# Performance work log

Measured on AMD Instinct MI355X. Metric: run time of the kernel, lower is better.

## Reference

```python
import jax, jax.numpy as jnp
import numpy as np

V = 32          # num_variables
T = 48          # num_time_bins
D = 512         # d_model
H = 8           # num_heads
HD = D // H     # head_dim = 64
OD = 16         # observation_dim
B = 4


def setup_inputs() -> dict:
    key = jax.random.key(0)
    ks = jax.random.split(key, 20)
    s = 0.02
    inp = {
        'h': jax.random.normal(ks[0], (B, T, V, D), jnp.float32),
        'observation_state': jax.random.normal(ks[1], (B, T, V, 2), jnp.float32),
        'Wq': jax.random.normal(ks[2], (D, D), jnp.float32) * s,
        'bq': jnp.zeros((D,), jnp.float32),
        'Wk': jax.random.normal(ks[3], (D, D), jnp.float32) * s,
        'bk': jnp.zeros((D,), jnp.float32),
        'Wv': jax.random.normal(ks[4], (D, D), jnp.float32) * s,
        'bv': jnp.zeros((D,), jnp.float32),
        'Wo': jax.random.normal(ks[5], (D, D), jnp.float32) * s,
        'bo': jnp.zeros((D,), jnp.float32),
        'Woq': jax.random.normal(ks[6], (2, H * OD), jnp.float32) * 0.5,
        'boq': jnp.zeros((H * OD,), jnp.float32),
        'Wok': jax.random.normal(ks[7], (2, H * OD), jnp.float32) * 0.5,
        'bok': jnp.zeros((H * OD,), jnp.float32),
        'variable_bias': jax.random.normal(ks[8], (H, V, V), jnp.float32) * 0.01,
        'relative_time_bias': jax.random.normal(ks[9], (H, 2 * T - 1), jnp.float32) * 0.01,
    }
    return inp


def reference(h, observation_state, Wq, bq, Wk, bk, Wv, bv, Wo, bo,
              Woq, boq, Wok, bok, variable_bias, relative_time_bias):
    N = T * V
    scale = 1.0 / np.sqrt(HD)
    obs_scale = 1.0 / np.sqrt(OD)

    # static index buffers (constants)
    flat_var_ids = jnp.tile(jnp.arange(V), T)                       # [N]
    flat_time_ids = jnp.repeat(jnp.arange(T), V)                    # [N]
    rel_index = flat_time_ids[:, None] - flat_time_ids[None, :] + (T - 1)  # [N,N]

    fh = h.reshape(B, N, D)
    fo = observation_state.reshape(B, N, 2)

    def heads(x, nh, hd):
        return x.reshape(B, N, nh, hd).transpose(0, 2, 1, 3)  # [B,H,N,hd]

    q = heads(fh @ Wq + bq, H, HD)
    k = heads(fh @ Wk + bk, H, HD)
    v = heads(fh @ Wv + bv, H, HD)
    oq = heads(fo @ Woq + boq, H, OD)
    ok = heads(fo @ Wok + bok, H, OD)

    content = jnp.einsum('bhnd,bhmd->bhnm', q, k) * scale
    obs = jnp.einsum('bhnd,bhmd->bhnm', oq, ok) * obs_scale
    var_scores = variable_bias[:, flat_var_ids[:, None], flat_var_ids[None, :]]  # [H,N,N]
    time_scores = relative_time_bias[:, rel_index]                                # [H,N,N]

    scores = content + obs + var_scores[None] + time_scores[None]
    attn = jax.nn.softmax(scores, axis=-1)  # dropout off (inference)
    out = jnp.einsum('bhnm,bhmd->bhnd', attn, v)
    out = out.transpose(0, 2, 1, 3).reshape(B, N, D)
    out = out @ Wo + bo
    return out.reshape(B, T, V, D)
```

## Files before the change

### kernel.cpp

```cpp
#include <hip/hip_runtime.h>
#include <math.h>

typedef __bf16 bf16x8 __attribute__((ext_vector_type(8)));
typedef float f32x4 __attribute__((ext_vector_type(4)));

#define NB 4
#define NT 48
#define NV 32
#define ND 512
#define NH 8
#define NN 1536
#define NBN 6144
#define L2E 1.44269504f

#define GLOAD_LDS(g, l) \
    __builtin_amdgcn_global_load_lds( \
        (const __attribute__((address_space(1))) void*)(g), \
        (__attribute__((address_space(3))) void*)(l), 16, 0, 0)

__global__ __launch_bounds__(256) void prep(
    const float* __restrict__ h, const float* __restrict__ obs,
    const float* __restrict__ Wq, const float* __restrict__ Wk,
    const float* __restrict__ Wv, const float* __restrict__ Wo,
    const float* __restrict__ bq, const float* __restrict__ bk,
    const float* __restrict__ bv,
    const float* __restrict__ Wok, const float* __restrict__ bok,
    __bf16* __restrict__ h_bf, __bf16* __restrict__ WcatT,
    __bf16* __restrict__ WoT, float* __restrict__ biascat,
    __bf16* __restrict__ kx)
{
    __shared__ float ts[64][68];
    const int tid = threadIdx.x;
    const int bx = blockIdx.x;
    if (bx < 1536) {
        int t = bx * 256 + tid;
        const float4* src = (const float4*)h + (size_t)t * 2;
        float4 a = src[0], b = src[1];
        __bf16 r[8] = {(__bf16)a.x, (__bf16)a.y, (__bf16)a.z, (__bf16)a.w,
                       (__bf16)b.x, (__bf16)b.y, (__bf16)b.z, (__bf16)b.w};
        *(uint4*)(h_bf + (size_t)t * 8) = *(uint4*)r;
    } else if (bx < 1792) {
        int bw = bx - 1536;
        const int p = bw >> 6, tile = bw & 63;
        const int k0 = (tile >> 3) * 64, c0 = (tile & 7) * 64;
        const float* W = (p == 0) ? Wq : (p == 1) ? Wk : (p == 2) ? Wv : Wo;
        const float scale = (p == 0) ? 0.125f * L2E : 1.0f;
        #pragma unroll
        for (int i = 0; i < 4; i++) {
            int r = (tid >> 4) + i * 16;
            float4 v = *(const float4*)(W + (size_t)(k0 + r) * 512 + c0 + (tid & 15) * 4);
            *(float4*)&ts[r][(tid & 15) * 4] = v;
        }
        __syncthreads();
        __bf16 tmp[16];
        #pragma unroll
        for (int j = 0; j < 16; j++)
            tmp[j] = (__bf16)(ts[(tid & 3) * 16 + j][tid >> 2] * scale);
        int crow = c0 + (tid >> 2);
        __bf16* dst = (p < 3)
            ? WcatT + ((size_t)(p * 512 + crow)) * 512 + k0 + (tid & 3) * 16
            : WoT   + ((size_t)crow) * 512 + k0 + (tid & 3) * 16;
        *(uint4*)dst = *(uint4*)tmp;
        *(uint4*)(dst + 8) = *(uint4*)(tmp + 8);
        if (p < 3 && k0 == 0 && tid < 64) {
            const float* bb = (p == 0) ? bq : (p == 1) ? bk : bv;
            biascat[p * 512 + c0 + tid] = bb[c0 + tid] * scale;
        }
    } else {
        int t = (bx - 1792) * 256 + tid;
        int row = t >> 1, half = t & 1;
        __bf16* dst = kx + (size_t)row * 96 + 64 + half * 16;
        if (half == 0) {
            int bh = row / NN, n = row - bh * NN;
            int b = bh >> 3, hh = bh & 7;
            size_t bn = (size_t)b * NN + n;
            float o0 = obs[bn * 2], o1 = obs[bn * 2 + 1];
            int f = hh * 16;
            __bf16 tmp[16];
            #pragma unroll
            for (int j = 0; j < 16; j++)
                tmp[j] = (__bf16)(o0 * Wok[f + j] + o1 * Wok[128 + f + j] + bok[f + j]);
            *(uint4*)dst       = *(uint4*)tmp;
            *(uint4*)(dst + 8) = *(uint4*)(tmp + 8);
        } else {
            uint4 z = {0, 0, 0, 0};
            *(uint4*)dst       = z;
            *(uint4*)(dst + 8) = z;
        }
    }
}

template<int TM, bool BF16OUT>
__global__ __launch_bounds__(256) void gemm_mfma(
    const __bf16* __restrict__ A, const __bf16* __restrict__ Bt,
    const float* __restrict__ bias, float* __restrict__ Cf,
    __bf16* __restrict__ qarr, __bf16* __restrict__ kx,
    __bf16* __restrict__ vt)
{
    constexpr int MT = TM / 32;
    __shared__ __align__(16) char smem[34816];
    char* const As0 = smem;
    char* const As1 = smem + TM * 64;
    char* const Bs0 = smem + TM * 128;
    char* const Bs1 = smem + TM * 128 + 8192;
    const int tid = threadIdx.x;
    const int w = tid >> 6, lane = tid & 63;
    const int quad = lane >> 4, l16 = lane & 15;
    const int wm = w >> 1, wn = w & 1;
    const int n0 = blockIdx.x * 128, m0 = blockIdx.y * TM;

    const int sm = tid >> 2;
    const int sk = ((tid & 3) ^ ((sm >> 1) & 3)) * 8;
    const __bf16* aptr = A  + (size_t)(m0 + sm) * 512 + sk;
    const __bf16* bptr = Bt + (size_t)(n0 + sm) * 512 + sk;

    f32x4 zero4 = {0.f, 0.f, 0.f, 0.f};
    f32x4 acc[MT][4];
    #pragma unroll
    for (int i = 0; i < MT; i++)
        #pragma unroll
        for (int j = 0; j < 4; j++) acc[i][j] = zero4;

    auto STAGE = [&](char* dA, char* dB, int kt) {
        GLOAD_LDS(aptr + kt, dA + tid * 16);
        if (TM == 128) GLOAD_LDS(aptr + 64 * 512 + kt, dA + 4096 + tid * 16);
        GLOAD_LDS(bptr + kt, dB + tid * 16);
        GLOAD_LDS(bptr + 64 * 512 + kt, dB + 4096 + tid * 16);
    };
    auto COMPUTE = [&](const char* Asb, const char* Bsb) {
        bf16x8 af[MT], bfr[4];
        #pragma unroll
        for (int mt = 0; mt < MT; mt++) {
            int rr = wm * (TM / 2) + mt * 16 + l16;
            af[mt] = *(const bf16x8*)(Asb + rr * 64 + (quad ^ ((rr >> 1) & 3)) * 16);
        }
        #pragma unroll
        for (int nt = 0; nt < 4; nt++) {
            int rr = wn * 64 + nt * 16 + l16;
            bfr[nt] = *(const bf16x8*)(Bsb + rr * 64 + (quad ^ ((rr >> 1) & 3)) * 16);
        }
        #pragma unroll
        for (int mt = 0; mt < MT; mt++)
            #pragma unroll
            for (int nt = 0; nt < 4; nt++)
                acc[mt][nt] = __builtin_amdgcn_mfma_f32_16x16x32_bf16(
                    af[mt], bfr[nt], acc[mt][nt], 0, 0, 0);
    };

    STAGE(As0, Bs0, 0);
    asm volatile("s_waitcnt vmcnt(0)" ::: "memory");
    __builtin_amdgcn_s_barrier();
    for (int kt = 0; kt < 512; kt += 64) {
        STAGE(As1, Bs1, kt + 32);
        COMPUTE(As0, Bs0);
        asm volatile("s_waitcnt vmcnt(0)" ::: "memory");
        __builtin_amdgcn_s_barrier();
        if (kt + 64 < 512) STAGE(As0, Bs0, kt + 64);
        COMPUTE(As1, Bs1);
        asm volatile("s_waitcnt vmcnt(0)" ::: "memory");
        __builtin_amdgcn_s_barrier();
    }

    __syncthreads();
    if (BF16OUT) {
        if (n0 >= 1024) {
            __bf16* CsT = (__bf16*)smem;
            #pragma unroll
            for (int nt = 0; nt < 4; nt++) {
                int cl = wn * 64 + nt * 16 + l16;
                float bia = bias[n0 + cl];
                #pragma unroll
                for (int mt = 0; mt < MT; mt++) {
                    int rl0 = wm * (TM / 2) + mt * 16 + quad * 4;
                    __bf16 pk[4];
                    #pragma unroll
                    for (int r = 0; r < 4; r++)
                        pk[r] = (__bf16)(acc[mt][nt][r] + bia);
                    *(uint2*)&CsT[cl * 136 + rl0] = *(uint2*)pk;
                }
            }
            __syncthreads();
            int cl = tid >> 1, half = tid & 1;
            int f0 = (n0 + cl) & 511;
            int hh = f0 >> 6, d = f0 & 63;
            int bidx = m0 / NN, nm = m0 - bidx * NN;
            __bf16* dst = vt + ((size_t)(bidx * 8 + hh) * 64 + d) * 1536
                             + nm + half * 64;
            #pragma unroll
            for (int j = 0; j < 8; j++) {
                uint4 v = *(uint4*)&CsT[cl * 136 + half * 64 + j * 8];
                *(uint4*)(dst + j * 8) = v;
            }
        } else {
            __bf16* Cs = (__bf16*)smem;
            #pragma unroll
            for (int mt = 0; mt < MT; mt++)
                #pragma unroll
                for (int nt = 0; nt < 4; nt++) {
                    int cl = wn * 64 + nt * 16 + l16;
                    float bia = bias[n0 + cl];
                    #pragma unroll
                    for (int r = 0; r < 4; r++) {
                        int rl = wm * (TM / 2) + mt * 16 + quad * 4 + r;
                        Cs[rl * 132 + cl] = (__bf16)(acc[mt][nt][r] + bia);
                    }
                }
            __syncthreads();
            int rl = tid >> 1, hb = tid & 1;
            int grow = m0 + rl;
            int col0 = n0 + hb * 64;
            int p = col0 >> 9, f0 = col0 & 511, hh = f0 >> 6;
            int bidx = grow / NN, n = grow - bidx * NN;
            __bf16* dst = (p == 0) ? qarr + (size_t)grow * 512 + f0
                                   : kx + ((size_t)(bidx * 8 + hh) * NN + n) * 96;
            #pragma unroll
            for (int j = 0; j < 8; j++) {
                uint2 lo = *(uint2*)&Cs[rl * 132 + hb * 64 + j * 8];
                uint2 hi = *(uint2*)&Cs[rl * 132 + hb * 64 + j * 8 + 4];
                uint4 v = {lo.x, lo.y, hi.x, hi.y};
                *(uint4*)(dst + j * 8) = v;
            }
        }
    } else {
        float* Csf = (float*)smem;
        #pragma unroll
        for (int mt = 0; mt < MT; mt++)
            #pragma unroll
            for (int nt = 0; nt < 4; nt++) {
                int cl = wn * 64 + nt * 16 + l16;
                float bia = bias[n0 + cl];
                #pragma unroll
                for (int r = 0; r < 4; r++) {
                    int rl = wm * (TM / 2) + mt * 16 + quad * 4 + r;
                    Csf[rl * 132 + cl] = acc[mt][nt][r] + bia;
                }
            }
        __syncthreads();
        int rl = tid >> 2, q4 = tid & 3;
        float* dst = Cf + (size_t)(m0 + rl) * 512 + n0 + q4 * 32;
        #pragma unroll
        for (int j = 0; j < 8; j++) {
            uint4 v = *(uint4*)&Csf[rl * 132 + q4 * 32 + j * 4];
            *(uint4*)(dst + j * 4) = v;
        }
    }
}

__global__ __launch_bounds__(256) void attn_mfma(
    const __bf16* __restrict__ qarr, const __bf16* __restrict__ kx,
    const __bf16* __restrict__ vt, const float* __restrict__ obs,
    const float* __restrict__ Woq, const float* __restrict__ boq,
    const float* __restrict__ varb, const float* __restrict__ rtb,
    __bf16* __restrict__ aout)
{
    __shared__ __align__(16) __bf16 Ks0[64][128];
    __shared__ __align__(16) __bf16 Ks1[64][128];
    __shared__ __align__(16) __bf16 Vs0[64][64];
    __shared__ __align__(16) __bf16 Vs1[64][64];
    __shared__ __align__(16) __bf16 Ps[64][64];
    __shared__ float rts[96];

    const int tid = threadIdx.x;
    const int w = tid >> 6, lane = tid & 63;
    const int quad = lane >> 4, l16 = lane & 15;
    const int bh = blockIdx.x, qt = blockIdx.y;
    const int b = bh >> 3, h = bh & 7;
    const int n0 = qt * 64;

    if (tid < 95) rts[tid] = rtb[h * 95 + tid] * L2E;

    const int ck = (tid & 15) ^ ((tid >> 4) & 7);
    const __bf16* kbase = kx + (size_t)bh * NN * 96 + ck * 8;
    const int cv = (tid & 7) ^ ((tid >> 3) & 7);
    const __bf16* vbase = vt + (size_t)bh * 64 * 1536 + cv * 8;

    auto STAGE = [&](char* dk, char* dv, int m0s) {
        #pragma unroll
        for (int i = 0; i < 4; i++) {
            int row = i * 16 + (tid >> 4);
            GLOAD_LDS(kbase + (size_t)(m0s + row) * 96, dk + i * 4096 + tid * 16);
        }
        #pragma unroll
        for (int i = 0; i < 2; i++) {
            int row = i * 32 + (tid >> 3);
            GLOAD_LDS(vbase + (size_t)row * 1536 + m0s, dv + i * 4096 + tid * 16);
        }
    };

    STAGE((char*)Ks0, (char*)Vs0, 0);

    const int nl = w * 16 + l16;
    const size_t qrow = (size_t)(b * NN + n0 + nl);
    bf16x8 bq_[3];
    bq_[0] = *(const bf16x8*)(qarr + qrow * 512 + h * 64 + quad * 8);
    bq_[1] = *(const bf16x8*)(qarr + qrow * 512 + h * 64 + 32 + quad * 8);
    {
        uint4 a2u = {0u, 0u, 0u, 0u};
        if (quad < 2) {
            float o0 = obs[qrow * 2], o1 = obs[qrow * 2 + 1];
            int f = h * 16 + quad * 8;
            const float sc = 0.25f * L2E;
            __bf16 tmp[8];
            #pragma unroll
            for (int j = 0; j < 8; j++)
                tmp[j] = (__bf16)(sc * (o0 * Woq[f + j] + o1 * Woq[128 + f + j]
                                        + boq[f + j]));
            a2u = *(uint4*)tmp;
        }
        bq_[2] = *(bf16x8*)&a2u;
    }

    const int rm = (w & 1) * 16 + l16;
    float4 vbA = *(const float4*)(varb + h * 1024 + rm * 32 + quad * 4);
    float4 vbB = *(const float4*)(varb + h * 1024 + rm * 32 + 16 + quad * 4);
    float vA[4] = {vbA.x * L2E, vbA.y * L2E, vbA.z * L2E, vbA.w * L2E};
    float vB[4] = {vbB.x * L2E, vbB.y * L2E, vbB.z * L2E, vbB.w * L2E};
    const int tn = 2 * qt + (w >> 1);

    int wo2[4], ro2[2];
    #pragma unroll
    for (int ct = 0; ct < 4; ct++)
        wo2[ct] = (((ct * 2 + (quad >> 1)) ^ (nl & 7)) * 16) + (quad & 1) * 8;
    #pragma unroll
    for (int ks = 0; ks < 2; ks++)
        ro2[ks] = ((ks * 4 + quad) ^ (nl & 7)) * 16;
    char* psrow = (char*)Ps + nl * 128;

    f32x4 zero4 = {0.f, 0.f, 0.f, 0.f};
    f32x4 o[4];
    f32x4 lpv = zero4;
    #pragma unroll
    for (int i = 0; i < 4; i++) o[i] = zero4;

    auto COMPUTE = [&](const char* Kb, const char* Vb, int mti) {
        f32x4 sc[4];
        __builtin_amdgcn_s_setprio(1);
        #pragma unroll
        for (int ct = 0; ct < 4; ct++) {
            f32x4 d = zero4;
            int row = ct * 16 + l16;
            #pragma unroll
            for (int ks = 0; ks < 3; ks++) {
                bf16x8 kf = *(const bf16x8*)(Kb + row * 256
                                + (((ks * 4 + quad) ^ (row & 7)) * 16));
                d = __builtin_amdgcn_mfma_f32_16x16x32_bf16(kf, bq_[ks], d, 0, 0, 0);
            }
            sc[ct] = d;
        }
        __builtin_amdgcn_s_setprio(0);
        float tb0 = rts[tn - 2 * mti + 47];
        float tb1 = rts[tn - 2 * mti + 46];
        #pragma unroll
        for (int ct = 0; ct < 4; ct++) {
            float tb = (ct & 2) ? tb1 : tb0;
            const float* vv = (ct & 1) ? vB : vA;
            __bf16 pk[4];
            #pragma unroll
            for (int r = 0; r < 4; r++) {
                float p = exp2f(sc[ct][r] + tb + vv[r]);
                lpv[r] += p;
                pk[r] = (__bf16)p;
            }
            *(uint2*)(psrow + wo2[ct]) = *(uint2*)pk;
        }
        __builtin_amdgcn_s_setprio(1);
        #pragma unroll
        for (int ks = 0; ks < 2; ks++) {
            bf16x8 pf = *(const bf16x8*)(psrow + ro2[ks]);
            #pragma unroll
            for (int dt = 0; dt < 4; dt++) {
                int rw = dt * 16 + l16;
                bf16x8 vf = *(const bf16x8*)(Vb + rw * 128
                                + (((ks * 4 + quad) ^ (rw & 7)) * 16));
                o[dt] = __builtin_amdgcn_mfma_f32_16x16x32_bf16(vf, pf, o[dt], 0, 0, 0);
            }
        }
        __builtin_amdgcn_s_setprio(0);
    };

    asm volatile("s_waitcnt vmcnt(0) lgkmcnt(0)" ::: "memory");
    __builtin_amdgcn_s_barrier();

    for (int mt = 0; mt < 24; mt += 2) {
        STAGE((char*)Ks1, (char*)Vs1, (mt + 1) * 64);
        COMPUTE((const char*)Ks0, (const char*)Vs0, mt);
        asm volatile("s_waitcnt vmcnt(0)" ::: "memory");
        __builtin_amdgcn_s_barrier();
        if (mt + 2 < 24) STAGE((char*)Ks0, (char*)Vs0, (mt + 2) * 64);
        COMPUTE((const char*)Ks1, (const char*)Vs1, mt + 1);
        asm volatile("s_waitcnt vmcnt(0)" ::: "memory");
        __builtin_amdgcn_s_barrier();
    }

    float lp = (lpv[0] + lpv[1]) + (lpv[2] + lpv[3]);
    lp += __shfl_xor(lp, 16);
    lp += __shfl_xor(lp, 32);
    float inv = 1.0f / lp;
    size_t abase = ((size_t)b * NN + n0 + nl) * 512 + h * 64 + quad * 4;
    #pragma unroll
    for (int dt = 0; dt < 4; dt++) {
        __bf16 ov[4];
        #pragma unroll
        for (int r = 0; r < 4; r++) ov[r] = (__bf16)(o[dt][r] * inv);
        *(uint2*)(aout + abase + dt * 16) = *(uint2*)ov;
    }
}

extern "C" void kernel_launch(void* const* d_in, const int* in_sizes, int n_in,
                              void* d_out, int out_size, void* d_ws, size_t ws_size,
                              hipStream_t stream)
{
    const float* h_   = (const float*)d_in[0];
    const float* obs  = (const float*)d_in[1];
    const float* Wq   = (const float*)d_in[2];
    const float* bq   = (const float*)d_in[3];
    const float* Wk   = (const float*)d_in[4];
    const float* bk   = (const float*)d_in[5];
    const float* Wv   = (const float*)d_in[6];
    const float* bv   = (const float*)d_in[7];
    const float* Wo   = (const float*)d_in[8];
    const float* bo   = (const float*)d_in[9];
    const float* Woq  = (const float*)d_in[10];
    const float* boq  = (const float*)d_in[11];
    const float* Wok  = (const float*)d_in[12];
    const float* bok  = (const float*)d_in[13];
    const float* varb = (const float*)d_in[14];
    const float* rtb  = (const float*)d_in[15];
    float* out = (float*)d_out;

    char* ws = (char*)d_ws;
    __bf16* h_bf    = (__bf16*)ws;                 ws += (size_t)NBN * 512 * 2;
    __bf16* qarr    = (__bf16*)ws;                 ws += (size_t)NBN * 512 * 2;
    __bf16* vt      = (__bf16*)ws;                 ws += (size_t)NBN * 512 * 2;
    __bf16* kx      = (__bf16*)ws;                 ws += ((size_t)32 * NN * 96 + 64) * 2;
    __bf16* attnout = (__bf16*)ws;                 ws += (size_t)NBN * 512 * 2;
    __bf16* WcatT   = (__bf16*)ws;                 ws += (size_t)1536 * 512 * 2;
    __bf16* WoT     = (__bf16*)ws;                 ws += (size_t)512 * 512 * 2;
    float*  biascat = (float*)ws;                  ws += 1536 * 4;

    prep<<<dim3(2176), dim3(256), 0, stream>>>(
        h_, obs, Wq, Wk, Wv, Wo, bq, bk, bv, Wok, bok,
        h_bf, WcatT, WoT, biascat, kx);
    gemm_mfma<128, true><<<dim3(12, 48), dim3(256), 0, stream>>>(
        h_bf, WcatT, biascat, nullptr, qarr, kx, vt);
    attn_mfma<<<dim3(32, 24), dim3(256), 0, stream>>>(qarr, kx, vt, obs, Woq, boq,
                                                      varb, rtb, attnout);
    gemm_mfma<64, false><<<dim3(4, 96), dim3(256), 0, stream>>>(
        attnout, WoT, bo, out, nullptr, nullptr, nullptr);
}
```

Measured before the change: 190.2 us.

## Single-buffer K tile in attention and issue next-tile loads after QK phase

Drops the second K shared-memory buffer and keeps double buffering only for V. The next K/V tile load is now issued after the QK MFMA phase and a barrier, instead of at the start of each iteration. This cuts LDS use by 16KB per block, which may allow more resident blocks per CU. In exchange it adds a barrier per tile and shortens the window in which the K load can overlap compute.

```diff
diff --git a/kernel.cpp b/kernel.cpp
--- a/kernel.cpp
+++ b/kernel.cpp
@@ -253,8 +253,7 @@
     const float* __restrict__ varb, const float* __restrict__ rtb,
     __bf16* __restrict__ aout)
 {
-    __shared__ __align__(16) __bf16 Ks0[64][128];
-    __shared__ __align__(16) __bf16 Ks1[64][128];
+    __shared__ __align__(16) __bf16 Ks[64][128];
     __shared__ __align__(16) __bf16 Vs0[64][64];
     __shared__ __align__(16) __bf16 Vs1[64][64];
     __shared__ __align__(16) __bf16 Ps[64][64];
@@ -274,12 +273,15 @@
     const int cv = (tid & 7) ^ ((tid >> 3) & 7);
     const __bf16* vbase = vt + (size_t)bh * 64 * 1536 + cv * 8;
 
-    auto STAGE = [&](char* dk, char* dv, int m0s) {
+    auto STAGE_K = [&](int m0s) {
         #pragma unroll
         for (int i = 0; i < 4; i++) {
             int row = i * 16 + (tid >> 4);
-            GLOAD_LDS(kbase + (size_t)(m0s + row) * 96, dk + i * 4096 + tid * 16);
-        }
+            GLOAD_LDS(kbase + (size_t)(m0s + row) * 96,
+                      (char*)Ks + i * 4096 + tid * 16);
+        }
+    };
+    auto STAGE_V = [&](char* dv, int m0s) {
         #pragma unroll
         for (int i = 0; i < 2; i++) {
             int row = i * 32 + (tid >> 3);
@@ -287,7 +289,8 @@
         }
     };
 
-    STAGE((char*)Ks0, (char*)Vs0, 0);
+    STAGE_K(0);
+    STAGE_V((char*)Vs0, 0);
 
     const int nl = w * 16 + l16;
     const size_t qrow = (size_t)(b * NN + n0 + nl);
@@ -332,7 +335,13 @@
     #pragma unroll
     for (int i = 0; i < 4; i++) o[i] = zero4;
 
-    auto COMPUTE = [&](const char* Kb, const char* Vb, int mti) {
+    asm volatile("s_waitcnt vmcnt(0) lgkmcnt(0)" ::: "memory");
+    __builtin_amdgcn_s_barrier();
+
+    const char* Vcur = (const char*)Vs0;
+    char* Vnxt = (char*)Vs1;
+
+    for (int mt = 0; mt < 24; mt++) {
         f32x4 sc[4];
         __builtin_amdgcn_s_setprio(1);
         #pragma unroll
@@ -341,15 +350,24 @@
             int row = ct * 16 + l16;
             #pragma unroll
             for (int ks = 0; ks < 3; ks++) {
-                bf16x8 kf = *(const bf16x8*)(Kb + row * 256
+                bf16x8 kf = *(const bf16x8*)((const char*)Ks + row * 256
                                 + (((ks * 4 + quad) ^ (row & 7)) * 16));
                 d = __builtin_amdgcn_mfma_f32_16x16x32_bf16(kf, bq_[ks], d, 0, 0, 0);
             }
             sc[ct] = d;
         }
         __builtin_amdgcn_s_setprio(0);
-        float tb0 = rts[tn - 2 * mti + 47];
-        float tb1 = rts[tn - 2 * mti + 46];
+
+        asm volatile("s_waitcnt lgkmcnt(0)" ::: "memory");
+        __builtin_amdgcn_s_barrier();
+
+        if (mt + 1 < 24) {
+            STAGE_K((mt + 1) * 64);
+            STAGE_V(Vnxt, (mt + 1) * 64);
+        }
+
+        float tb0 = rts[tn - 2 * mt + 47];
+        float tb1 = rts[tn - 2 * mt + 46];
         #pragma unroll
         for (int ct = 0; ct < 4; ct++) {
             float tb = (ct & 2) ? tb1 : tb0;
@@ -363,6 +381,7 @@
             }
             *(uint2*)(psrow + wo2[ct]) = *(uint2*)pk;
         }
+
         __builtin_amdgcn_s_setprio(1);
         #pragma unroll
         for (int ks = 0; ks < 2; ks++) {
@@ -370,26 +389,17 @@
             #pragma unroll
             for (int dt = 0; dt < 4; dt++) {
                 int rw = dt * 16 + l16;
-                bf16x8 vf = *(const bf16x8*)(Vb + rw * 128
+                bf16x8 vf = *(const bf16x8*)(Vcur + rw * 128
                                 + (((ks * 4 + quad) ^ (rw & 7)) * 16));
                 o[dt] = __builtin_amdgcn_mfma_f32_16x16x32_bf16(vf, pf, o[dt], 0, 0, 0);
             }
         }
         __builtin_amdgcn_s_setprio(0);
-    };
-
-    asm volatile("s_waitcnt vmcnt(0) lgkmcnt(0)" ::: "memory");
-    __builtin_amdgcn_s_barrier();
-
-    for (int mt = 0; mt < 24; mt += 2) {
-        STAGE((char*)Ks1, (char*)Vs1, (mt + 1) * 64);
-        COMPUTE((const char*)Ks0, (const char*)Vs0, mt);
+
         asm volatile("s_waitcnt vmcnt(0)" ::: "memory");
         __builtin_amdgcn_s_barrier();
-        if (mt + 2 < 24) STAGE((char*)Ks0, (char*)Vs0, (mt + 2) * 64);
-        COMPUTE((const char*)Ks1, (const char*)Vs1, mt + 1);
-        asm volatile("s_waitcnt vmcnt(0)" ::: "memory");
-        __builtin_amdgcn_s_barrier();
+
+        const char* t = Vcur; Vcur = (const char*)Vnxt; Vnxt = (char*)t;
     }
 
     float lp = (lpv[0] + lpv[1]) + (lpv[2] + lpv[3]);
```

New measurement: 184.2 us. 3.2% less time.
